# Kernel optimization log

Hardware: AMD Instinct MI355X
Metric: run time of the kernel (lower is better)

Reference implementation:

```python
import jax, jax.numpy as jnp
import numpy as np

B, NWORD, HID = 4, 24, 512


def setup_inputs() -> dict:
    key = jax.random.key(0)
    ks = jax.random.split(key, 7)
    H = HID
    scale_in = 1.0 / np.sqrt(H)
    return {
        "seqt": jax.random.normal(ks[0], (B, NWORD, 2 * H), dtype=jnp.float32),
        # ins_input_linearity: Linear(H -> 5H) with bias
        "Wi": jax.random.normal(ks[1], (5 * H, H), dtype=jnp.float32) * scale_in,
        "bi": jnp.zeros((5 * H,), dtype=jnp.float32),
        # ins_state_linearity: Linear(H -> 5H) with bias (bias init: forget slots = 1)
        "Ws": jax.random.normal(ks[2], (5 * H, H), dtype=jnp.float32) * scale_in,
        "bs": jnp.zeros((5 * H,), dtype=jnp.float32).at[H:2 * H].set(1.0),
        # ins_bilinearity: BilinearSimilarity(2H, 2H) -> scalar x^T W y
        "Wbil": jax.random.normal(ks[3], (2 * H, 2 * H), dtype=jnp.float32) * (1.0 / (2.0 * H)),
    }


def reference(seqt, Wi, bi, Ws, bs, Wbil):
    """Inside pass (do_inside) of DioLstm in training mode (soft_sum over splits).

    Chart cell (left, L) covers words [left, left+L]. Returns root v = concat(h, c).
    """
    Bn, n, twoH = seqt.shape
    H = twoH // 2
    # ins_bias buffer: ones on the two forget-gate slots [H:3H]
    ins_bias = jnp.zeros((5 * H,), dtype=seqt.dtype).at[H:3 * H].set(1.0)

    def single(seq):  # seq: [n, 2H]
        chartH = jnp.zeros((n, n, H), seq.dtype).at[:, 0].set(seq[:, :H])
        chartC = jnp.zeros((n, n, H), seq.dtype).at[:, 0].set(seq[:, H:])
        chartS = jnp.zeros((n, n), seq.dtype)  # leaf scores are 0
        for L in range(1, n):  # span length - 1 (static unroll over diagonals)
            P = n - L  # number of spans on this diagonal
            lefts = jnp.arange(P)[:, None]          # [P,1]
            ksplit = jnp.arange(L)[None, :]          # [1,L]
            # left child: (left, k); right child: (left+k+1, L-1-k)
            lH = chartH[lefts, ksplit]; lC = chartC[lefts, ksplit]; lS = chartS[lefts, ksplit]
            ridx = lefts + ksplit + 1
            rlen = jnp.broadcast_to(L - 1 - ksplit, ridx.shape)
            rH = chartH[ridx, rlen]; rC = chartC[ridx, rlen]; rS = chartS[ridx, rlen]
            lv = jnp.concatenate([lH, lC], axis=-1)  # [P,L,2H]
            rv = jnp.concatenate([rH, rC], axis=-1)
            # bilinear compatibility + child scores
            compat = jnp.einsum('pki,ij,pkj->pk', lv, Wbil, rv) + lS + rS  # [P,L]
            # projected_input + projected_state (sum once; gate slices of the sum)
            proj = (lH @ Wi.T + bi + ins_bias) + (rH @ Ws.T + bs)  # [P,L,5H]
            ig, lf, rf, g, og = jnp.split(proj, 5, axis=-1)
            ig = jax.nn.sigmoid(ig); lf = jax.nn.sigmoid(lf); rf = jax.nn.sigmoid(rf)
            g = jnp.tanh(g); og = jax.nn.sigmoid(og)
            mem = lf * lC + rf * rC + ig * g
            h = og * jnp.tanh(mem)  # [P,L,H]
            # soft_sum: torch.tensor(s_set) detaches scores -> stop_gradient on weights
            sw = jax.lax.stop_gradient(compat)
            w = jax.nn.softmax(sw, axis=-1)  # [P,L]
            Hnew = jnp.einsum('pk,pkh->ph', w, h)
            Cnew = jnp.einsum('pk,pkh->ph', w, mem)
            Snew = jnp.sum(w * sw, axis=-1)
            pidx = jnp.arange(P)
            chartH = chartH.at[pidx, L].set(Hnew)
            chartC = chartC.at[pidx, L].set(Cnew)
            chartS = chartS.at[pidx, L].set(Snew)
        # root cell v = concat(h, c)
        return jnp.concatenate([chartH[0, n - 1], chartC[0, n - 1]], axis=0)

    return jax.vmap(single)(seqt)  # [B, 2H]
```

## Files before the change

### kernel.cpp

```cpp
#include <hip/hip_runtime.h>
#include <math.h>

#define NB 4
#define NW 24
#define H 512
#define H2 1024
#define H5 2560
#define NCELL 300
#define NEED_BYTES ((size_t)72<<20)

static float* g_buf = nullptr;
__attribute__((constructor)) static void dio_alloc_ws(){
  (void)hipMalloc((void**)&g_buf, NEED_BYTES);
}

typedef __attribute__((ext_vector_type(8))) short bf16x8;
typedef __attribute__((ext_vector_type(4))) float f32x4;
typedef unsigned short ushort_t;

__device__ __forceinline__ int coff(int l){ return l*NW - (l*(l-1))/2; }
__device__ __forceinline__ float sigm(float x){ return 1.f/(1.f+__expf(-x)); }
__device__ __forceinline__ float ftanh(float x){ return 1.f - 2.f/(__expf(2.f*x)+1.f); }

__device__ __forceinline__ ushort_t f2b(float x){
  unsigned int u = __float_as_uint(x);
  u += 0x7FFF + ((u>>16)&1);
  return (ushort_t)(u>>16);
}
__device__ __forceinline__ float b2f(ushort_t h){
  return __uint_as_float(((unsigned int)h)<<16);
}
__device__ __forceinline__ void split_store(ushort_t* __restrict__ ph,
                                            ushort_t* __restrict__ pl,
                                            size_t idx, float x){
  ushort_t h = f2b(x);
  ph[idx] = h;
  pl[idx] = f2b(x - b2f(h));
}

__device__ __forceinline__ float compat_dot(const float* __restrict__ cU,
                                            const float* __restrict__ cH,
                                            const float* __restrict__ cC,
                                            const float* __restrict__ cS,
                                            int lc, int rc, int lane){
  const float4* U4  = (const float4*)(cU + (size_t)lc*H2);
  const float4* Hr4 = (const float4*)(cH + (size_t)rc*H);
  const float4* Cr4 = (const float4*)(cC + (size_t)rc*H);
  float p = 0.f;
  #pragma unroll
  for (int it=0; it<2; it++){
    float4 u = U4[lane + 64*it], h = Hr4[lane + 64*it];
    p += u.x*h.x + u.y*h.y + u.z*h.z + u.w*h.w;
  }
  #pragma unroll
  for (int it=0; it<2; it++){
    float4 u = U4[128 + lane + 64*it], c = Cr4[lane + 64*it];
    p += u.x*c.x + u.y*c.y + u.z*c.z + u.w*c.w;
  }
  #pragma unroll
  for (int off=32; off>0; off>>=1) p += __shfl_down(p, off);
  return p + cS[lc] + cS[rc];
}

__global__ void k_init(const float* __restrict__ seqt,
                       const float* __restrict__ Wi, const float* __restrict__ Ws,
                       const float* __restrict__ Wbil,
                       ushort_t* __restrict__ WiBh, ushort_t* __restrict__ WiBl,
                       ushort_t* __restrict__ WsBh, ushort_t* __restrict__ WsBl,
                       ushort_t* __restrict__ WbilTh, ushort_t* __restrict__ WbilTl,
                       float* __restrict__ cH, float* __restrict__ cC, float* __restrict__ cS,
                       ushort_t* __restrict__ cHbh, ushort_t* __restrict__ cHbl,
                       ushort_t* __restrict__ cCbh, ushort_t* __restrict__ cCbl){
  const int blk = blockIdx.x, t = threadIdx.x;
  if (blk < 10240){
    int i = blk*256 + t;
    const int n = H5*H;
    if (i < n) split_store(WiBh, WiBl, i, Wi[i]);
    else       split_store(WsBh, WsBl, i-n, Ws[i-n]);
  } else if (blk < 11264){
    __shared__ float tile[32][33];
    int tb = blk - 10240;
    int tr = (tb>>5)*32, tc = (tb&31)*32;
    int tx = t & 31, ty = t >> 5;
    #pragma unroll
    for (int i=0;i<32;i+=8)
      tile[ty+i][tx] = Wbil[(size_t)(tr+ty+i)*H2 + tc+tx];
    __syncthreads();
    #pragma unroll
    for (int i=0;i<32;i+=8)
      split_store(WbilTh, WbilTl, (size_t)(tc+ty+i)*H2 + tr+tx, tile[tx][ty+i]);
  } else {
    int tid = (blk-11264)*256 + t;
    if (tid < NB*NW*H){
      int b = tid/(NW*H); int r = tid%(NW*H); int i = r/H; int d = r%H;
      size_t idx = (size_t)(b*NCELL + i)*H + d;
      float hv = seqt[(size_t)(b*NW+i)*H2 + d];
      float cv = seqt[(size_t)(b*NW+i)*H2 + H + d];
      cH[idx]=hv; cC[idx]=cv;
      split_store(cHbh,cHbl,idx,hv);
      split_store(cCbh,cCbl,idx,cv);
      if (d==0) cS[b*NCELL+i] = 0.f;
    }
  }
}

__device__ __forceinline__ void mfma3(f32x4& acc, bf16x8 ah, bf16x8 al,
                                      bf16x8 bh, bf16x8 bl){
  acc = __builtin_amdgcn_mfma_f32_16x16x32_bf16(ah, bh, acc, 0,0,0);
  acc = __builtin_amdgcn_mfma_f32_16x16x32_bf16(ah, bl, acc, 0,0,0);
  acc = __builtin_amdgcn_mfma_f32_16x16x32_bf16(al, bh, acc, 0,0,0);
}

__global__ void __launch_bounds__(512)
k_proj2(const ushort_t* __restrict__ WiBh, const ushort_t* __restrict__ WiBl,
        const ushort_t* __restrict__ WsBh, const ushort_t* __restrict__ WsBl,
        const ushort_t* __restrict__ WbilTh, const ushort_t* __restrict__ WbilTl,
        const float* __restrict__ bi, const float* __restrict__ bs,
        const ushort_t* __restrict__ cHbh, const ushort_t* __restrict__ cHbl,
        const ushort_t* __restrict__ cCbh, const ushort_t* __restrict__ cCbl,
        float* __restrict__ cPI, float* __restrict__ cPS, float* __restrict__ cU,
        int d, int P)
{
  __shared__ __attribute__((aligned(16))) ushort_t wlds[32768];
  __shared__ f32x4 red[8][64];
  const int t = threadIdx.x, wv = t>>6, lane = t&63;
  const int r = lane & 15;
  const int q = lane >> 4;
  const int jt = blockIdx.x;

  int kind, j0;
  if (jt < 160){ kind=0; j0 = jt*16; }
  else if (jt < 320){ kind=1; j0 = (jt-160)*16; }
  else { kind=2; j0 = (jt-320)*16; }

  char* wb = (char*)wlds;
  if (kind < 2){
    const ushort_t* srcH = (kind==0 ? WiBh : WsBh) + (size_t)j0*H;
    const ushort_t* srcL = (kind==0 ? WiBl : WsBl) + (size_t)j0*H;
    #pragma unroll
    for (int e = t; e < 1024; e += 512){
      const int row = e >> 6, c0 = (e & 63) << 3;
      bf16x8 vh = *(const bf16x8*)(srcH + (size_t)row*H + c0);
      bf16x8 vl = *(const bf16x8*)(srcL + (size_t)row*H + c0);
      const int off = ((row<<10) + (c0<<1)) ^ ((row&7)<<4);
      *(bf16x8*)(wb + off) = vh;
      *(bf16x8*)(wb + 16384 + off) = vl;
    }
  } else {
    const ushort_t* srcH = WbilTh + (size_t)j0*H2;
    const ushort_t* srcL = WbilTl + (size_t)j0*H2;
    #pragma unroll
    for (int e = t; e < 2048; e += 512){
      const int row = e >> 7, c0 = (e & 127) << 3;
      bf16x8 vh = *(const bf16x8*)(srcH + (size_t)row*H2 + c0);
      bf16x8 vl = *(const bf16x8*)(srcL + (size_t)row*H2 + c0);
      const int off = ((row<<11) + (c0<<1)) ^ ((row&7)<<4);
      *(bf16x8*)(wb + off) = vh;
      *(bf16x8*)(wb + 32768 + off) = vl;
    }
  }
  __syncthreads();

  const int Mtot = NB*P, mt = (Mtot+15)>>4;
  const int swz = (r&7)<<4;
  const int jo = j0 + r;
  float bias = 0.f;
  if (kind==0) bias = bi[jo] + ((jo>=H && jo<3*H)?1.f:0.f);
  else if (kind==1) bias = bs[jo];

  const f32x4 z4 = {0.f,0.f,0.f,0.f};
  const int units = 2*mt;
  const int rounds = (units + 7) >> 3;
  for (int rd = 0; rd < rounds; rd++){
    const int u = rd*8 + wv;
    const int half = u & 1;
    const int mtile = u >> 1;
    f32x4 sA = z4;
    int m0 = 0, nm = 0;
    if (u < units){
      m0 = mtile*16;
      nm = min(16, Mtot - m0);
      const int mg = m0 + (r < nm ? r : 0);
      const size_t arow = (size_t)((mg/P)*NCELL + coff(d) + mg%P)*H;
      f32x4 acc[4];
      #pragma unroll
      for (int wi=0;wi<4;wi++) acc[wi] = z4;
      if (kind < 2){
        #pragma unroll
        for (int wi=0; wi<4; wi++){
          const int w = half*4 + wi;
          #pragma unroll
          for (int s=0;s<2;s++){
            const int ko = w*64 + q*8 + s*32;
            bf16x8 ah = *(const bf16x8*)(cHbh + arow + ko);
            bf16x8 al = *(const bf16x8*)(cHbl + arow + ko);
            const int bo = ((r<<10) + (ko<<1)) ^ swz;
            bf16x8 bh = *(const bf16x8*)(wb + bo);
            bf16x8 bl = *(const bf16x8*)(wb + 16384 + bo);
            mfma3(acc[wi], ah, al, bh, bl);
          }
        }
      } else {
        const ushort_t* ah_ = (half==0 ? cHbh : cCbh) + arow;
        const ushort_t* al_ = (half==0 ? cHbl : cCbl) + arow;
        #pragma unroll
        for (int wi=0; wi<4; wi++){
          const int w = half*4 + wi;
          const int kg0 = w*128, ka0 = kg0 & 511;
          #pragma unroll
          for (int s=0;s<4;s++){
            const int so = s*32 + q*8;
            bf16x8 ah = *(const bf16x8*)(ah_ + ka0 + so);
            bf16x8 al = *(const bf16x8*)(al_ + ka0 + so);
            const int bo = ((r<<11) + ((kg0+so)<<1)) ^ swz;
            bf16x8 bh = *(const bf16x8*)(wb + bo);
            bf16x8 bl = *(const bf16x8*)(wb + 32768 + bo);
            mfma3(acc[wi], ah, al, bh, bl);
          }
        }
      }
      sA = (acc[0]+acc[1]) + (acc[2]+acc[3]);
    }
    red[wv][lane] = sA;
    __syncthreads();
    if (half==0 && u < units){
      f32x4 tot = red[wv][lane] + red[wv|1][lane];
      #pragma unroll
      for (int reg=0; reg<4; reg++){
        const int m = q*4 + reg;
        if (m < nm){
          const int mg2 = m0 + m;
          const size_t cell = (size_t)((mg2/P)*NCELL + coff(d) + mg2%P);
          const float v = tot[reg];
          if (kind==0)      cPI[cell*H5 + jo] = v + bias;
          else if (kind==1) cPS[cell*H5 + jo] = v + bias;
          else              cU [cell*H2 + jo] = v;
        }
      }
    }
    __syncthreads();
  }
}

__global__ void __launch_bounds__(256)
k_combine3(const float* __restrict__ cPI, const float* __restrict__ cPS,
           const float* __restrict__ cU,
           float* __restrict__ cH, float* __restrict__ cC, float* __restrict__ cS,
           ushort_t* __restrict__ cHbh, ushort_t* __restrict__ cHbl,
           ushort_t* __restrict__ cCbh, ushort_t* __restrict__ cCbl,
           const float* __restrict__ compatR, float* __restrict__ compatW,
           int L, int P){
  const int t = threadIdx.x;
  const int lane = t & 63;
  const int wave = t >> 6;
  const int nphase = NB*P*16;
  const int blk = blockIdx.x;

  if (blk >= nphase){
    const int P1 = P-1;
    const int nterm = L-1;
    int tid = (blk-nphase)*4 + wave;
    if (P1 > 0 && nterm > 0 && tid < NB*P1*nterm){
      int cell1 = tid / nterm;
      int k = 1 + tid % nterm;
      int b = cell1 / P1, left = cell1 % P1;
      int lc = b*NCELL + coff(k) + left;
      int rc = b*NCELL + coff(L-k) + left+k+1;
      float v = compat_dot(cU, cH, cC, cS, lc, rc, lane);
      if (lane==0) compatW[(b*NW + left)*NW + k] = v;
    }
    return;
  }

  const int cellid = blk >> 4;
  const int dg = blk & 15;
  const int b = cellid / P;
  const int left = cellid % P;
  __shared__ float compat_s[32];
  __shared__ float wts_s[32];
  __shared__ float S_s;
  __shared__ float partH[8][32];
  __shared__ float partC[8][32];

  if (wave == 0){
    int lc = b*NCELL + left;
    int rc = b*NCELL + coff(L-1) + left+1;
    float v = compat_dot(cU, cH, cC, cS, lc, rc, lane);
    if (lane==0) compat_s[0] = v;
  } else if (wave == 1 && L >= 2){
    int lc = b*NCELL + coff(L-1) + left;
    int rc = b*NCELL + left+L;
    float v = compat_dot(cU, cH, cC, cS, lc, rc, lane);
    if (lane==0) compat_s[L-1] = v;
  }
  if (t >= 1 && t <= L-2) compat_s[t] = compatR[(b*NW + left)*NW + t];
  __syncthreads();
  if (t==0){
    float mx = -1e30f;
    for (int k=0;k<L;k++) mx = fmaxf(mx, compat_s[k]);
    float den = 0.f;
    for (int k=0;k<L;k++){ float e = __expf(compat_s[k]-mx); wts_s[k]=e; den+=e; }
    float inv = 1.f/den, S = 0.f;
    for (int k=0;k<L;k++){ wts_s[k]*=inv; S += wts_s[k]*compat_s[k]; }
    S_s = S;
  }
  __syncthreads();
  const int dloc = t & 31;
  const int dim = dg*32 + dloc;
  const int kpar = t >> 5;
  float aH = 0.f, aC = 0.f;
  for (int k=kpar; k<L; k+=8){
    float wk = wts_s[k];
    int lc = b*NCELL + coff(k) + left;
    int rc = b*NCELL + coff(L-1-k) + left+k+1;
    const float* PI = cPI + (size_t)lc*H5;
    const float* PS = cPS + (size_t)rc*H5;
    float p0 = PI[dim]     + PS[dim];
    float p1 = PI[H+dim]   + PS[H+dim];
    float p2 = PI[2*H+dim] + PS[2*H+dim];
    float p3 = PI[3*H+dim] + PS[3*H+dim];
    float p4 = PI[4*H+dim] + PS[4*H+dim];
    float lcv = cC[(size_t)lc*H + dim];
    float rcv = cC[(size_t)rc*H + dim];
    float mem = sigm(p1)*lcv + sigm(p2)*rcv + sigm(p0)*ftanh(p3);
    float h = sigm(p4)*ftanh(mem);
    aH += wk*h; aC += wk*mem;
  }
  if (kpar > 0){ partH[kpar][dloc]=aH; partC[kpar][dloc]=aC; }
  __syncthreads();
  if (kpar == 0){
    #pragma unroll
    for (int q=1;q<8;q++){ aH += partH[q][dloc]; aC += partC[q][dloc]; }
    size_t nc = (size_t)(b*NCELL + coff(L) + left);
    cH[nc*H + dim] = aH;
    cC[nc*H + dim] = aC;
    split_store(cHbh,cHbl, nc*H + dim, aH);
    split_store(cCbh,cCbl, nc*H + dim, aC);
    if (t==0 && dg==0) cS[nc] = S_s;
  }
}

__global__ void k_out(const float* __restrict__ cH, const float* __restrict__ cC,
                      float* __restrict__ out){
  int tid = blockIdx.x*256+threadIdx.x;
  if (tid >= NB*H2) return;
  int b = tid>>10, d = tid&1023;
  int cell = b*NCELL + 299;
  out[tid] = (d<H) ? cH[(size_t)cell*H + d] : cC[(size_t)cell*H + (d-H)];
}

extern "C" void kernel_launch(void* const* d_in, const int* in_sizes, int n_in,
                              void* d_out, int out_size, void* d_ws, size_t ws_size,
                              hipStream_t stream){
  const float* seqt = (const float*)d_in[0];
  const float* Wi   = (const float*)d_in[1];
  const float* bi   = (const float*)d_in[2];
  const float* Ws   = (const float*)d_in[3];
  const float* bs   = (const float*)d_in[4];
  const float* Wbil = (const float*)d_in[5];
  float* out = (float*)d_out;

  float* p = (ws_size >= NEED_BYTES && g_buf == nullptr) ? (float*)d_ws : g_buf;
  float* cH  = p; p += (size_t)NB*NCELL*H;
  float* cC  = p; p += (size_t)NB*NCELL*H;
  float* cS  = p; p += (size_t)NB*NCELL;
  float* cPI = p; p += (size_t)NB*NCELL*H5;
  float* cPS = p; p += (size_t)NB*NCELL*H5;
  float* cU  = p; p += (size_t)NB*NCELL*H2;
  float* compatA = p; p += (size_t)NB*NW*NW;
  float* compatB = p; p += (size_t)NB*NW*NW;
  ushort_t* u = (ushort_t*)p;
  ushort_t* WiBh   = u; u += (size_t)H5*H;
  ushort_t* WiBl   = u; u += (size_t)H5*H;
  ushort_t* WsBh   = u; u += (size_t)H5*H;
  ushort_t* WsBl   = u; u += (size_t)H5*H;
  ushort_t* WbilTh = u; u += (size_t)H2*H2;
  ushort_t* WbilTl = u; u += (size_t)H2*H2;
  ushort_t* cHbh   = u; u += (size_t)NB*NCELL*H;
  ushort_t* cHbl   = u; u += (size_t)NB*NCELL*H;
  ushort_t* cCbh   = u; u += (size_t)NB*NCELL*H;
  ushort_t* cCbl   = u; u += (size_t)NB*NCELL*H;

  k_init<<<11456, 256, 0, stream>>>(seqt, Wi, Ws, Wbil,
      WiBh, WiBl, WsBh, WsBl, WbilTh, WbilTl,
      cH, cC, cS, cHbh, cHbl, cCbh, cCbl);

  k_proj2<<<384, 512, 0, stream>>>(
      WiBh, WiBl, WsBh, WsBl, WbilTh, WbilTl, bi, bs,
      cHbh, cHbl, cCbh, cCbl, cPI, cPS, cU, 0, NW);
  for (int L=1; L<NW; L++){
    int P = NW - L;
    int P1 = P-1, nterm = L-1;
    int wblk = (P1>0 && nterm>0) ? (NB*P1*nterm + 3)/4 : 0;
    float* bufR = (L&1) ? compatA : compatB;
    float* bufW = (L&1) ? compatB : compatA;
    k_combine3<<<NB*P*16 + wblk, 256, 0, stream>>>(
        cPI, cPS, cU, cH, cC, cS, cHbh, cHbl, cCbh, cCbl,
        bufR, bufW, L, P);
    if (L < NW-1)
      k_proj2<<<384, 512, 0, stream>>>(
          WiBh, WiBl, WsBh, WsBl, WbilTh, WbilTl, bi, bs,
          cHbh, cHbl, cCbh, cCbl, cPI, cPS, cU, L, P);
  }
  k_out<<<16, 256, 0, stream>>>(cH, cC, out);
}
```

Baseline: 584.1 us.

## Fuse combine and projection into one per-diagonal kernel with flag-based handoff

Merges the per-diagonal combine kernel and the projection GEMM kernel into a single launch per diagonal. Projection blocks spin on per-cell flags set by combine blocks, so the GEMM can start on rows as soon as they are written instead of waiting for a kernel boundary. This also folds the output copy into the last stage. The combine now uses one 512-thread block per cell rather than sixteen 256-thread blocks. It risks deadlock if projection blocks occupy the CUs before the combine blocks are scheduled, and adds atomic-load overhead on the A fragments.

New measurement: 883.3 us. 1.51x slower.

```diff
diff --git a/kernel.cpp b/kernel.cpp
--- a/kernel.cpp
+++ b/kernel.cpp
@@ -17,6 +17,7 @@
 typedef __attribute__((ext_vector_type(8))) short bf16x8;
 typedef __attribute__((ext_vector_type(4))) float f32x4;
 typedef unsigned short ushort_t;
+typedef unsigned long long u64_t;
 
 __device__ __forceinline__ int coff(int l){ return l*NW - (l*(l-1))/2; }
 __device__ __forceinline__ float sigm(float x){ return 1.f/(1.f+__expf(-x)); }
@@ -36,6 +37,14 @@
   ushort_t h = f2b(x);
   ph[idx] = h;
   pl[idx] = f2b(x - b2f(h));
+}
+
+__device__ __forceinline__ bf16x8 ld_frag_agent(const ushort_t* p){
+  u64_t a = __hip_atomic_load((u64_t*)p,     __ATOMIC_RELAXED, __HIP_MEMORY_SCOPE_AGENT);
+  u64_t b = __hip_atomic_load((u64_t*)p + 1, __ATOMIC_RELAXED, __HIP_MEMORY_SCOPE_AGENT);
+  union { u64_t q[2]; bf16x8 v; } u;
+  u.q[0] = a; u.q[1] = b;
+  return u.v;
 }
 
 __device__ __forceinline__ float compat_dot(const float* __restrict__ cU,
@@ -70,7 +79,8 @@
                        ushort_t* __restrict__ WbilTh, ushort_t* __restrict__ WbilTl,
                        float* __restrict__ cH, float* __restrict__ cC, float* __restrict__ cS,
                        ushort_t* __restrict__ cHbh, ushort_t* __restrict__ cHbl,
-                       ushort_t* __restrict__ cCbh, ushort_t* __restrict__ cCbl){
+                       ushort_t* __restrict__ cCbh, ushort_t* __restrict__ cCbl,
+                       unsigned* __restrict__ flags){
   const int blk = blockIdx.x, t = threadIdx.x;
   if (blk < 10240){
     int i = blk*256 + t;
@@ -89,7 +99,7 @@
     #pragma unroll
     for (int i=0;i<32;i+=8)
       split_store(WbilTh, WbilTl, (size_t)(tc+ty+i)*H2 + tr+tx, tile[tx][ty+i]);
-  } else {
+  } else if (blk < 11456){
     int tid = (blk-11264)*256 + t;
     if (tid < NB*NW*H){
       int b = tid/(NW*H); int r = tid%(NW*H); int i = r/H; int d = r%H;
@@ -101,6 +111,8 @@
       split_store(cCbh,cCbl,idx,cv);
       if (d==0) cS[b*NCELL+i] = 0.f;
     }
+  } else {
+    for (int i=t; i<NW*128; i+=256) flags[i] = 0u;
   }
 }
 
@@ -112,21 +124,129 @@
 }
 
 __global__ void __launch_bounds__(512)
-k_proj2(const ushort_t* __restrict__ WiBh, const ushort_t* __restrict__ WiBl,
+k_stage(const ushort_t* __restrict__ WiBh, const ushort_t* __restrict__ WiBl,
         const ushort_t* __restrict__ WsBh, const ushort_t* __restrict__ WsBl,
         const ushort_t* __restrict__ WbilTh, const ushort_t* __restrict__ WbilTl,
         const float* __restrict__ bi, const float* __restrict__ bs,
-        const ushort_t* __restrict__ cHbh, const ushort_t* __restrict__ cHbl,
-        const ushort_t* __restrict__ cCbh, const ushort_t* __restrict__ cCbl,
+        ushort_t* cHbh, ushort_t* cHbl, ushort_t* cCbh, ushort_t* cCbl,
         float* __restrict__ cPI, float* __restrict__ cPS, float* __restrict__ cU,
-        int d, int P)
+        float* __restrict__ cH, float* __restrict__ cC, float* __restrict__ cS,
+        const float* __restrict__ compatR, float* __restrict__ compatW,
+        unsigned* flags, float* __restrict__ out, int L)
 {
   __shared__ __attribute__((aligned(16))) ushort_t wlds[32768];
   __shared__ f32x4 red[8][64];
-  const int t = threadIdx.x, wv = t>>6, lane = t&63;
+  __shared__ float compat_s[32];
+  __shared__ float wts_s[32];
+
+  const int P = NW - L;
+  const int ncomb = (L>=1) ? NB*P : 0;
+  const int P1 = P-1, nterm = L-1;
+  const int nwt = (L>=1 && P1>0 && nterm>0) ? NB*P1*nterm : 0;
+  const int wblkN = (nwt+7)>>3;
+  const int t = threadIdx.x, wave = t>>6, lane = t&63;
+  unsigned* flagD = flags + L*128;
+  int blk = blockIdx.x;
+
+  if (blk < ncomb){
+    const int b = blk / P, left = blk % P;
+    if (wave == 4){
+      int lc = b*NCELL + left;
+      int rc = b*NCELL + coff(L-1) + left+1;
+      float v = compat_dot(cU, cH, cC, cS, lc, rc, lane);
+      if (lane==0) compat_s[0] = v;
+    } else if (wave == 5 && L >= 2){
+      int lc = b*NCELL + coff(L-1) + left;
+      int rc = b*NCELL + left+L;
+      float v = compat_dot(cU, cH, cC, cS, lc, rc, lane);
+      if (lane==0) compat_s[L-1] = v;
+    }
+    if (t >= 1 && t <= L-2) compat_s[t] = compatR[(b*NW + left)*NW + t];
+    __syncthreads();
+    const size_t nc = (size_t)(b*NCELL + coff(L) + left);
+    if (t==0){
+      float mx = -1e30f;
+      for (int k=0;k<L;k++) mx = fmaxf(mx, compat_s[k]);
+      float den = 0.f;
+      for (int k=0;k<L;k++){ float e = __expf(compat_s[k]-mx); wts_s[k]=e; den+=e; }
+      float inv = 1.f/den, S = 0.f;
+      for (int k=0;k<L;k++){ wts_s[k]*=inv; S += wts_s[k]*compat_s[k]; }
+      if (L < NW-1) cS[nc] = S;
+    }
+    __syncthreads();
+    const int dim = t;
+    float aH = 0.f, aC = 0.f;
+    for (int q8=0; q8<8; q8++){
+      float sH = 0.f, sC = 0.f;
+      for (int k=q8; k<L; k+=8){
+        float wk = wts_s[k];
+        int lc = b*NCELL + coff(k) + left;
+        int rc = b*NCELL + coff(L-1-k) + left+k+1;
+        const float* PI = cPI + (size_t)lc*H5;
+        const float* PS = cPS + (size_t)rc*H5;
+        float p0 = PI[dim]     + PS[dim];
+        float p1 = PI[H+dim]   + PS[H+dim];
+        float p2 = PI[2*H+dim] + PS[2*H+dim];
+        float p3 = PI[3*H+dim] + PS[3*H+dim];
+        float p4 = PI[4*H+dim] + PS[4*H+dim];
+        float lcv = cC[(size_t)lc*H + dim];
+        float rcv = cC[(size_t)rc*H + dim];
+        float mem = sigm(p1)*lcv + sigm(p2)*rcv + sigm(p0)*ftanh(p3);
+        float h = sigm(p4)*ftanh(mem);
+        sH += wk*h; sC += wk*mem;
+      }
+      aH += sH; aC += sC;
+    }
+    if (L == NW-1){
+      out[b*H2 + dim]     = aH;
+      out[b*H2 + H + dim] = aC;
+      return;
+    }
+    cH[nc*H + dim] = aH;
+    cC[nc*H + dim] = aC;
+    ushort_t hH = f2b(aH), lH = f2b(aH - b2f(hH));
+    ushort_t hC = f2b(aC), lC = f2b(aC - b2f(hC));
+    unsigned nh = (unsigned)__shfl_down((int)hH, 1);
+    unsigned nl = (unsigned)__shfl_down((int)lH, 1);
+    unsigned mh = (unsigned)__shfl_down((int)hC, 1);
+    unsigned ml = (unsigned)__shfl_down((int)lC, 1);
+    if (!(t & 1)){
+      const size_t pi = (nc*H + dim) >> 1;
+      __hip_atomic_store((unsigned*)cHbh + pi, (unsigned)hH | (nh<<16),
+                         __ATOMIC_RELAXED, __HIP_MEMORY_SCOPE_AGENT);
+      __hip_atomic_store((unsigned*)cHbl + pi, (unsigned)lH | (nl<<16),
+                         __ATOMIC_RELAXED, __HIP_MEMORY_SCOPE_AGENT);
+      __hip_atomic_store((unsigned*)cCbh + pi, (unsigned)hC | (mh<<16),
+                         __ATOMIC_RELAXED, __HIP_MEMORY_SCOPE_AGENT);
+      __hip_atomic_store((unsigned*)cCbl + pi, (unsigned)lC | (ml<<16),
+                         __ATOMIC_RELAXED, __HIP_MEMORY_SCOPE_AGENT);
+    }
+    __syncthreads();
+    if (t == 0)
+      __hip_atomic_fetch_add(flagD + b*32 + left, 1u,
+                             __ATOMIC_RELAXED, __HIP_MEMORY_SCOPE_AGENT);
+    return;
+  }
+  blk -= ncomb;
+
+  if (blk < wblkN){
+    const int tid8 = blk*8 + wave;
+    if (tid8 < nwt){
+      int cell1 = tid8 / nterm;
+      int k = 1 + tid8 % nterm;
+      int b = cell1 / P1, left = cell1 % P1;
+      int lc = b*NCELL + coff(k) + left;
+      int rc = b*NCELL + coff(L-k) + left+k+1;
+      float v = compat_dot(cU, cH, cC, cS, lc, rc, lane);
+      if (lane==0) compatW[(b*NW + left)*NW + k] = v;
+    }
+    return;
+  }
+  blk -= wblkN;
+
+  const int jt = blk;
   const int r = lane & 15;
   const int q = lane >> 4;
-  const int jt = blockIdx.x;
 
   int kind, j0;
   if (jt < 160){ kind=0; j0 = jt*16; }
@@ -172,7 +292,18 @@
   const int units = 2*mt;
   const int rounds = (units + 7) >> 3;
   for (int rd = 0; rd < rounds; rd++){
-    const int u = rd*8 + wv;
+    if (L >= 1){
+      const int c0 = rd*64;
+      const int c1 = min(Mtot, c0+64);
+      if (t < c1 - c0){
+        const int mg = c0 + t;
+        unsigned* f = flagD + (mg/P)*32 + (mg%P);
+        while (__hip_atomic_load(f, __ATOMIC_RELAXED, __HIP_MEMORY_SCOPE_AGENT) == 0u)
+          __builtin_amdgcn_s_sleep(2);
+      }
+      __syncthreads();
+    }
+    const int u = rd*8 + wave;
     const int half = u & 1;
     const int mtile = u >> 1;
     f32x4 sA = z4;
@@ -181,7 +312,7 @@
       m0 = mtile*16;
       nm = min(16, Mtot - m0);
       const int mg = m0 + (r < nm ? r : 0);
-      const size_t arow = (size_t)((mg/P)*NCELL + coff(d) + mg%P)*H;
+      const size_t arow = (size_t)((mg/P)*NCELL + coff(L) + mg%P)*H;
       f32x4 acc[4];
       #pragma unroll
       for (int wi=0;wi<4;wi++) acc[wi] = z4;
@@ -192,8 +323,8 @@
           #pragma unroll
           for (int s=0;s<2;s++){
             const int ko = w*64 + q*8 + s*32;
-            bf16x8 ah = *(const bf16x8*)(cHbh + arow + ko);
-            bf16x8 al = *(const bf16x8*)(cHbl + arow + ko);
+            bf16x8 ah = ld_frag_agent(cHbh + arow + ko);
+            bf16x8 al = ld_frag_agent(cHbl + arow + ko);
             const int bo = ((r<<10) + (ko<<1)) ^ swz;
             bf16x8 bh = *(const bf16x8*)(wb + bo);
             bf16x8 bl = *(const bf16x8*)(wb + 16384 + bo);
@@ -210,8 +341,8 @@
           #pragma unroll
           for (int s=0;s<4;s++){
             const int so = s*32 + q*8;
-            bf16x8 ah = *(const bf16x8*)(ah_ + ka0 + so);
-            bf16x8 al = *(const bf16x8*)(al_ + ka0 + so);
+            bf16x8 ah = ld_frag_agent(ah_ + ka0 + so);
+            bf16x8 al = ld_frag_agent(al_ + ka0 + so);
             const int bo = ((r<<11) + ((kg0+so)<<1)) ^ swz;
             bf16x8 bh = *(const bf16x8*)(wb + bo);
             bf16x8 bl = *(const bf16x8*)(wb + 32768 + bo);
@@ -221,16 +352,16 @@
       }
       sA = (acc[0]+acc[1]) + (acc[2]+acc[3]);
     }
-    red[wv][lane] = sA;
+    red[wave][lane] = sA;
     __syncthreads();
     if (half==0 && u < units){
-      f32x4 tot = red[wv][lane] + red[wv|1][lane];
+      f32x4 tot = red[wave][lane] + red[wave|1][lane];
       #pragma unroll
       for (int reg=0; reg<4; reg++){
         const int m = q*4 + reg;
         if (m < nm){
           const int mg2 = m0 + m;
-          const size_t cell = (size_t)((mg2/P)*NCELL + coff(d) + mg2%P);
+          const size_t cell = (size_t)((mg2/P)*NCELL + coff(L) + mg2%P);
           const float v = tot[reg];
           if (kind==0)      cPI[cell*H5 + jo] = v + bias;
           else if (kind==1) cPS[cell*H5 + jo] = v + bias;
@@ -240,113 +371,6 @@
     }
     __syncthreads();
   }
-}
-
-__global__ void __launch_bounds__(256)
-k_combine3(const float* __restrict__ cPI, const float* __restrict__ cPS,
-           const float* __restrict__ cU,
-           float* __restrict__ cH, float* __restrict__ cC, float* __restrict__ cS,
-           ushort_t* __restrict__ cHbh, ushort_t* __restrict__ cHbl,
-           ushort_t* __restrict__ cCbh, ushort_t* __restrict__ cCbl,
-           const float* __restrict__ compatR, float* __restrict__ compatW,
-           int L, int P){
-  const int t = threadIdx.x;
-  const int lane = t & 63;
-  const int wave = t >> 6;
-  const int nphase = NB*P*16;
-  const int blk = blockIdx.x;
-
-  if (blk >= nphase){
-    const int P1 = P-1;
-    const int nterm = L-1;
-    int tid = (blk-nphase)*4 + wave;
-    if (P1 > 0 && nterm > 0 && tid < NB*P1*nterm){
-      int cell1 = tid / nterm;
-      int k = 1 + tid % nterm;
-      int b = cell1 / P1, left = cell1 % P1;
-      int lc = b*NCELL + coff(k) + left;
-      int rc = b*NCELL + coff(L-k) + left+k+1;
-      float v = compat_dot(cU, cH, cC, cS, lc, rc, lane);
-      if (lane==0) compatW[(b*NW + left)*NW + k] = v;
-    }
-    return;
-  }
-
-  const int cellid = blk >> 4;
-  const int dg = blk & 15;
-  const int b = cellid / P;
-  const int left = cellid % P;
-  __shared__ float compat_s[32];
-  __shared__ float wts_s[32];
-  __shared__ float S_s;
-  __shared__ float partH[8][32];
-  __shared__ float partC[8][32];
-
-  if (wave == 0){
-    int lc = b*NCELL + left;
-    int rc = b*NCELL + coff(L-1) + left+1;
-    float v = compat_dot(cU, cH, cC, cS, lc, rc, lane);
-    if (lane==0) compat_s[0] = v;
-  } else if (wave == 1 && L >= 2){
-    int lc = b*NCELL + coff(L-1) + left;
-    int rc = b*NCELL + left+L;
-    float v = compat_dot(cU, cH, cC, cS, lc, rc, lane);
-    if (lane==0) compat_s[L-1] = v;
-  }
-  if (t >= 1 && t <= L-2) compat_s[t] = compatR[(b*NW + left)*NW + t];
-  __syncthreads();
-  if (t==0){
-    float mx = -1e30f;
-    for (int k=0;k<L;k++) mx = fmaxf(mx, compat_s[k]);
-    float den = 0.f;
-    for (int k=0;k<L;k++){ float e = __expf(compat_s[k]-mx); wts_s[k]=e; den+=e; }
-    float inv = 1.f/den, S = 0.f;
-    for (int k=0;k<L;k++){ wts_s[k]*=inv; S += wts_s[k]*compat_s[k]; }
-    S_s = S;
-  }
-  __syncthreads();
-  const int dloc = t & 31;
-  const int dim = dg*32 + dloc;
-  const int kpar = t >> 5;
-  float aH = 0.f, aC = 0.f;
-  for (int k=kpar; k<L; k+=8){
-    float wk = wts_s[k];
-    int lc = b*NCELL + coff(k) + left;
-    int rc = b*NCELL + coff(L-1-k) + left+k+1;
-    const float* PI = cPI + (size_t)lc*H5;
-    const float* PS = cPS + (size_t)rc*H5;
-    float p0 = PI[dim]     + PS[dim];
-    float p1 = PI[H+dim]   + PS[H+dim];
-    float p2 = PI[2*H+dim] + PS[2*H+dim];
-    float p3 = PI[3*H+dim] + PS[3*H+dim];
-    float p4 = PI[4*H+dim] + PS[4*H+dim];
-    float lcv = cC[(size_t)lc*H + dim];
-    float rcv = cC[(size_t)rc*H + dim];
-    float mem = sigm(p1)*lcv + sigm(p2)*rcv + sigm(p0)*ftanh(p3);
-    float h = sigm(p4)*ftanh(mem);
-    aH += wk*h; aC += wk*mem;
-  }
-  if (kpar > 0){ partH[kpar][dloc]=aH; partC[kpar][dloc]=aC; }
-  __syncthreads();
-  if (kpar == 0){
-    #pragma unroll
-    for (int q=1;q<8;q++){ aH += partH[q][dloc]; aC += partC[q][dloc]; }
-    size_t nc = (size_t)(b*NCELL + coff(L) + left);
-    cH[nc*H + dim] = aH;
-    cC[nc*H + dim] = aC;
-    split_store(cHbh,cHbl, nc*H + dim, aH);
-    split_store(cCbh,cCbl, nc*H + dim, aC);
-    if (t==0 && dg==0) cS[nc] = S_s;
-  }
-}
-
-__global__ void k_out(const float* __restrict__ cH, const float* __restrict__ cC,
-                      float* __restrict__ out){
-  int tid = blockIdx.x*256+threadIdx.x;
-  if (tid >= NB*H2) return;
-  int b = tid>>10, d = tid&1023;
-  int cell = b*NCELL + 299;
-  out[tid] = (d<H) ? cH[(size_t)cell*H + d] : cC[(size_t)cell*H + (d-H)];
 }
 
 extern "C" void kernel_launch(void* const* d_in, const int* in_sizes, int n_in,
@@ -380,27 +404,24 @@
   ushort_t* cHbl   = u; u += (size_t)NB*NCELL*H;
   ushort_t* cCbh   = u; u += (size_t)NB*NCELL*H;
   ushort_t* cCbl   = u; u += (size_t)NB*NCELL*H;
-
-  k_init<<<11456, 256, 0, stream>>>(seqt, Wi, Ws, Wbil,
+  unsigned* flags  = (unsigned*)u;
+
+  k_init<<<11457, 256, 0, stream>>>(seqt, Wi, Ws, Wbil,
       WiBh, WiBl, WsBh, WsBl, WbilTh, WbilTl,
-      cH, cC, cS, cHbh, cHbl, cCbh, cCbl);
-
-  k_proj2<<<384, 512, 0, stream>>>(
-      WiBh, WiBl, WsBh, WsBl, WbilTh, WbilTl, bi, bs,
-      cHbh, cHbl, cCbh, cCbl, cPI, cPS, cU, 0, NW);
-  for (int L=1; L<NW; L++){
+      cH, cC, cS, cHbh, cHbl, cCbh, cCbl, flags);
+
+  for (int L=0; L<NW; L++){
     int P = NW - L;
+    int ncomb = (L>=1) ? NB*P : 0;
     int P1 = P-1, nterm = L-1;
-    int wblk = (P1>0 && nterm>0) ? (NB*P1*nterm + 3)/4 : 0;
+    int nwt = (L>=1 && P1>0 && nterm>0) ? NB*P1*nterm : 0;
+    int wblk = (nwt+7)>>3;
+    int nproj = (L <= NW-2) ? 384 : 0;
     float* bufR = (L&1) ? compatA : compatB;
     float* bufW = (L&1) ? compatB : compatA;
-    k_combine3<<<NB*P*16 + wblk, 256, 0, stream>>>(
-        cPI, cPS, cU, cH, cC, cS, cHbh, cHbl, cCbh, cCbl,
-        bufR, bufW, L, P);
-    if (L < NW-1)
-      k_proj2<<<384, 512, 0, stream>>>(
-          WiBh, WiBl, WsBh, WsBl, WbilTh, WbilTl, bi, bs,
-          cHbh, cHbl, cCbh, cCbl, cPI, cPS, cU, L, P);
-  }
-  k_out<<<16, 256, 0, stream>>>(cH, cC, out);
-}
+    k_stage<<<ncomb + wblk + nproj, 512, 0, stream>>>(
+        WiBh, WiBl, WsBh, WsBl, WbilTh, WbilTl, bi, bs,
+        cHbh, cHbl, cCbh, cCbl, cPI, cPS, cU, cH, cC, cS,
+        bufR, bufW, flags, out, L);
+  }
+}
```

## Pre-swizzle weight tiles into LDS-ready blobs and load via global_load_lds

Applied to the files above, without the earlier changes.

The init kernel now writes the split bf16 hi/lo weights into per-tile contiguous blobs that already use the swizzled LDS layout, vectorizing the conversion eight elements per thread. The projection kernel then fills LDS with direct global-to-LDS 16-byte loads instead of register round-trips and per-row address math. The final combine step writes the root cell straight to the output, removing the separate output kernel launch. This relies on the blob layout matching the LDS swizzle exactly and on global_load_lds wave-contiguous addressing.

Measured after the change: 577.9 us. No clear change (-1.1%).

```diff
diff --git a/kernel.cpp b/kernel.cpp
--- a/kernel.cpp
+++ b/kernel.cpp
@@ -36,6 +36,12 @@
   ushort_t h = f2b(x);
   ph[idx] = h;
   pl[idx] = f2b(x - b2f(h));
+}
+
+__device__ __forceinline__ void gload_lds16(const void* g, void* l){
+  __builtin_amdgcn_global_load_lds(
+      (const __attribute__((address_space(1))) unsigned int*)g,
+      (__attribute__((address_space(3))) unsigned int*)l, 16, 0, 0);
 }
 
 __device__ __forceinline__ float compat_dot(const float* __restrict__ cU,
@@ -65,32 +71,61 @@
 __global__ void k_init(const float* __restrict__ seqt,
                        const float* __restrict__ Wi, const float* __restrict__ Ws,
                        const float* __restrict__ Wbil,
-                       ushort_t* __restrict__ WiBh, ushort_t* __restrict__ WiBl,
-                       ushort_t* __restrict__ WsBh, ushort_t* __restrict__ WsBl,
-                       ushort_t* __restrict__ WbilTh, ushort_t* __restrict__ WbilTl,
+                       ushort_t* __restrict__ WWblob, ushort_t* __restrict__ WBblob,
                        float* __restrict__ cH, float* __restrict__ cC, float* __restrict__ cS,
                        ushort_t* __restrict__ cHbh, ushort_t* __restrict__ cHbl,
                        ushort_t* __restrict__ cCbh, ushort_t* __restrict__ cCbl){
   const int blk = blockIdx.x, t = threadIdx.x;
-  if (blk < 10240){
-    int i = blk*256 + t;
-    const int n = H5*H;
-    if (i < n) split_store(WiBh, WiBl, i, Wi[i]);
-    else       split_store(WsBh, WsBl, i-n, Ws[i-n]);
-  } else if (blk < 11264){
+  if (blk < 1280){
+    const int gid = blk*256 + t;
+    const int half = 163840;
+    const float* mat = (gid < half) ? Wi : Ws;
+    const int cid = (gid < half) ? gid : gid - half;
+    const int j = cid >> 6;
+    const int c0 = (cid & 63) << 3;
+    const int tile = ((gid < half) ? 0 : 160) + (j >> 4);
+    const int row = j & 15;
+    const float4* s = (const float4*)(mat + (size_t)j*H + c0);
+    float4 a = s[0], b4 = s[1];
+    float xs[8] = {a.x,a.y,a.z,a.w, b4.x,b4.y,b4.z,b4.w};
+    union { ushort_t u[8]; bf16x8 v; } hh, ll;
+    #pragma unroll
+    for (int i=0;i<8;i++){
+      ushort_t h = f2b(xs[i]);
+      hh.u[i] = h; ll.u[i] = f2b(xs[i] - b2f(h));
+    }
+    char* base = (char*)WWblob + (size_t)tile*32768;
+    const int off = ((row<<10) + (c0<<1)) ^ ((row&7)<<4);
+    *(bf16x8*)(base + off) = hh.v;
+    *(bf16x8*)(base + 16384 + off) = ll.v;
+  } else if (blk < 2304){
     __shared__ float tile[32][33];
-    int tb = blk - 10240;
+    int tb = blk - 1280;
     int tr = (tb>>5)*32, tc = (tb&31)*32;
     int tx = t & 31, ty = t >> 5;
     #pragma unroll
     for (int i=0;i<32;i+=8)
       tile[ty+i][tx] = Wbil[(size_t)(tr+ty+i)*H2 + tc+tx];
     __syncthreads();
-    #pragma unroll
-    for (int i=0;i<32;i+=8)
-      split_store(WbilTh, WbilTl, (size_t)(tc+ty+i)*H2 + tr+tx, tile[tx][ty+i]);
+    if (t < 128){
+      const int c = t & 31, r0 = (t >> 5) << 3;
+      const int jg = tc + c;
+      const int k0 = tr + r0;
+      union { ushort_t u[8]; bf16x8 v; } hh, ll;
+      #pragma unroll
+      for (int i=0;i<8;i++){
+        float x = tile[r0+i][c];
+        ushort_t h = f2b(x);
+        hh.u[i] = h; ll.u[i] = f2b(x - b2f(h));
+      }
+      char* base = (char*)WBblob + (size_t)(jg>>4)*65536;
+      const int row = jg & 15;
+      const int off = ((row<<11) + (k0<<1)) ^ ((row&7)<<4);
+      *(bf16x8*)(base + off) = hh.v;
+      *(bf16x8*)(base + 32768 + off) = ll.v;
+    }
   } else {
-    int tid = (blk-11264)*256 + t;
+    int tid = (blk-2304)*256 + t;
     if (tid < NB*NW*H){
       int b = tid/(NW*H); int r = tid%(NW*H); int i = r/H; int d = r%H;
       size_t idx = (size_t)(b*NCELL + i)*H + d;
@@ -112,9 +147,7 @@
 }
 
 __global__ void __launch_bounds__(512)
-k_proj2(const ushort_t* __restrict__ WiBh, const ushort_t* __restrict__ WiBl,
-        const ushort_t* __restrict__ WsBh, const ushort_t* __restrict__ WsBl,
-        const ushort_t* __restrict__ WbilTh, const ushort_t* __restrict__ WbilTl,
+k_proj3(const ushort_t* __restrict__ WWblob, const ushort_t* __restrict__ WBblob,
         const float* __restrict__ bi, const float* __restrict__ bs,
         const ushort_t* __restrict__ cHbh, const ushort_t* __restrict__ cHbl,
         const ushort_t* __restrict__ cCbh, const ushort_t* __restrict__ cCbl,
@@ -133,36 +166,22 @@
   else if (jt < 320){ kind=1; j0 = (jt-160)*16; }
   else { kind=2; j0 = (jt-320)*16; }
 
-  char* wb = (char*)wlds;
-  if (kind < 2){
-    const ushort_t* srcH = (kind==0 ? WiBh : WsBh) + (size_t)j0*H;
-    const ushort_t* srcL = (kind==0 ? WiBl : WsBl) + (size_t)j0*H;
-    #pragma unroll
-    for (int e = t; e < 1024; e += 512){
-      const int row = e >> 6, c0 = (e & 63) << 3;
-      bf16x8 vh = *(const bf16x8*)(srcH + (size_t)row*H + c0);
-      bf16x8 vl = *(const bf16x8*)(srcL + (size_t)row*H + c0);
-      const int off = ((row<<10) + (c0<<1)) ^ ((row&7)<<4);
-      *(bf16x8*)(wb + off) = vh;
-      *(bf16x8*)(wb + 16384 + off) = vl;
-    }
-  } else {
-    const ushort_t* srcH = WbilTh + (size_t)j0*H2;
-    const ushort_t* srcL = WbilTl + (size_t)j0*H2;
-    #pragma unroll
-    for (int e = t; e < 2048; e += 512){
-      const int row = e >> 7, c0 = (e & 127) << 3;
-      bf16x8 vh = *(const bf16x8*)(srcH + (size_t)row*H2 + c0);
-      bf16x8 vl = *(const bf16x8*)(srcL + (size_t)row*H2 + c0);
-      const int off = ((row<<11) + (c0<<1)) ^ ((row&7)<<4);
-      *(bf16x8*)(wb + off) = vh;
-      *(bf16x8*)(wb + 32768 + off) = vl;
-    }
+  {
+    const char* blob = (kind < 2)
+        ? (const char*)WWblob + (size_t)jt*32768
+        : (const char*)WBblob + (size_t)(jt-320)*65536;
+    const int nseg = (kind < 2) ? 4 : 8;
+    for (int i = 0; i < nseg; i++){
+      const int lo = i*8192 + wv*1024;
+      gload_lds16(blob + lo + lane*16, (char*)wlds + lo);
+    }
+    asm volatile("s_waitcnt vmcnt(0)" ::: "memory");
   }
   __syncthreads();
 
   const int Mtot = NB*P, mt = (Mtot+15)>>4;
   const int swz = (r&7)<<4;
+  const char* wb = (const char*)wlds;
   const int jo = j0 + r;
   float bias = 0.f;
   if (kind==0) bias = bi[jo] + ((jo>=H && jo<3*H)?1.f:0.f);
@@ -249,7 +268,7 @@
            ushort_t* __restrict__ cHbh, ushort_t* __restrict__ cHbl,
            ushort_t* __restrict__ cCbh, ushort_t* __restrict__ cCbl,
            const float* __restrict__ compatR, float* __restrict__ compatW,
-           int L, int P){
+           float* __restrict__ out, int L, int P){
   const int t = threadIdx.x;
   const int lane = t & 63;
   const int wave = t >> 6;
@@ -331,6 +350,11 @@
   if (kpar == 0){
     #pragma unroll
     for (int q=1;q<8;q++){ aH += partH[q][dloc]; aC += partC[q][dloc]; }
+    if (L == NW-1){
+      out[b*H2 + dim]     = aH;
+      out[b*H2 + H + dim] = aC;
+      return;
+    }
     size_t nc = (size_t)(b*NCELL + coff(L) + left);
     cH[nc*H + dim] = aH;
     cC[nc*H + dim] = aC;
@@ -338,15 +362,6 @@
     split_store(cCbh,cCbl, nc*H + dim, aC);
     if (t==0 && dg==0) cS[nc] = S_s;
   }
-}
-
-__global__ void k_out(const float* __restrict__ cH, const float* __restrict__ cC,
-                      float* __restrict__ out){
-  int tid = blockIdx.x*256+threadIdx.x;
-  if (tid >= NB*H2) return;
-  int b = tid>>10, d = tid&1023;
-  int cell = b*NCELL + 299;
-  out[tid] = (d<H) ? cH[(size_t)cell*H + d] : cC[(size_t)cell*H + (d-H)];
 }
 
 extern "C" void kernel_launch(void* const* d_in, const int* in_sizes, int n_in,
@@ -370,23 +385,18 @@
   float* compatA = p; p += (size_t)NB*NW*NW;
   float* compatB = p; p += (size_t)NB*NW*NW;
   ushort_t* u = (ushort_t*)p;
-  ushort_t* WiBh   = u; u += (size_t)H5*H;
-  ushort_t* WiBl   = u; u += (size_t)H5*H;
-  ushort_t* WsBh   = u; u += (size_t)H5*H;
-  ushort_t* WsBl   = u; u += (size_t)H5*H;
-  ushort_t* WbilTh = u; u += (size_t)H2*H2;
-  ushort_t* WbilTl = u; u += (size_t)H2*H2;
+  ushort_t* WWblob = u; u += (size_t)320*16384;
+  ushort_t* WBblob = u; u += (size_t)64*32768;
   ushort_t* cHbh   = u; u += (size_t)NB*NCELL*H;
   ushort_t* cHbl   = u; u += (size_t)NB*NCELL*H;
   ushort_t* cCbh   = u; u += (size_t)NB*NCELL*H;
   ushort_t* cCbl   = u; u += (size_t)NB*NCELL*H;
 
-  k_init<<<11456, 256, 0, stream>>>(seqt, Wi, Ws, Wbil,
-      WiBh, WiBl, WsBh, WsBl, WbilTh, WbilTl,
-      cH, cC, cS, cHbh, cHbl, cCbh, cCbl);
-
-  k_proj2<<<384, 512, 0, stream>>>(
-      WiBh, WiBl, WsBh, WsBl, WbilTh, WbilTl, bi, bs,
+  k_init<<<2496, 256, 0, stream>>>(seqt, Wi, Ws, Wbil,
+      WWblob, WBblob, cH, cC, cS, cHbh, cHbl, cCbh, cCbl);
+
+  k_proj3<<<384, 512, 0, stream>>>(
+      WWblob, WBblob, bi, bs,
       cHbh, cHbl, cCbh, cCbl, cPI, cPS, cU, 0, NW);
   for (int L=1; L<NW; L++){
     int P = NW - L;
@@ -396,11 +406,10 @@
     float* bufW = (L&1) ? compatB : compatA;
     k_combine3<<<NB*P*16 + wblk, 256, 0, stream>>>(
         cPI, cPS, cU, cH, cC, cS, cHbh, cHbl, cCbh, cCbl,
-        bufR, bufW, L, P);
+        bufR, bufW, out, L, P);
     if (L < NW-1)
-      k_proj2<<<384, 512, 0, stream>>>(
-          WiBh, WiBl, WsBh, WsBl, WbilTh, WbilTl, bi, bs,
+      k_proj3<<<384, 512, 0, stream>>>(
+          WWblob, WBblob, bi, bs,
           cHbh, cHbl, cCbh, cCbl, cPI, cPS, cU, L, P);
   }
-  k_out<<<16, 256, 0, stream>>>(cH, cC, out);
-}
+}
```
